# Kernel optimization log

Hardware: AMD Instinct MI355X
Metric: run time of the kernel (lower is better)

## Reference

```python
import jax, jax.numpy as jnp
import numpy as np

GN_GROUPS = 32
EPS = 1e-5
GRADIENT_MUL = 0.1
DCN_K = 3
DCN_PAD = 1


def conv(x, w, b=None, pad=0):
    out = jax.lax.conv_general_dilated(x, w, (1, 1), [(pad, pad), (pad, pad)],
                                       dimension_numbers=('NCHW', 'OIHW', 'NCHW'))
    if b is not None:
        out = out + b[None, :, None, None]
    return out


def group_norm(x, gamma, beta):
    B, C, H, W = x.shape
    xg = x.reshape(B, GN_GROUPS, C // GN_GROUPS, H, W)
    mu = xg.mean(axis=(2, 3, 4), keepdims=True)
    var = xg.var(axis=(2, 3, 4), keepdims=True)
    xg = (xg - mu) * jax.lax.rsqrt(var + EPS)
    return xg.reshape(B, C, H, W) * gamma[None, :, None, None] + beta[None, :, None, None]


def dcn_base_offset():
    base = np.arange(-DCN_PAD, DCN_PAD + 1, dtype=np.float32)
    y = np.repeat(base, DCN_K)
    x = np.tile(base, DCN_K)
    return jnp.asarray(np.stack([y, x], 1).reshape(1, -1, 1, 1))  # [1,2K,1,1], (y,x) interleaved


def deform_conv(x, offset, weight):
    # x [B,C,H,W]; offset [B,2K,H,W] (y,x) interleaved per kernel point; weight [O,C,3,3]
    B, C, H, W = x.shape
    K = DCN_K * DCN_K
    off = offset.reshape(B, K, 2, H, W)
    base = jnp.arange(DCN_K, dtype=x.dtype) - DCN_PAD
    ky = jnp.repeat(base, DCN_K)
    kx = jnp.tile(base, DCN_K)
    gy = jnp.arange(H, dtype=x.dtype)[None, None, :, None] + ky[None, :, None, None] + off[:, :, 0]
    gx = jnp.arange(W, dtype=x.dtype)[None, None, None, :] + kx[None, :, None, None] + off[:, :, 1]
    y0 = jnp.floor(gy)
    x0 = jnp.floor(gx)
    dy = gy - y0
    dx = gx - x0

    def corner(yi, xi, wgt):
        valid = (yi >= 0) & (yi < H) & (xi >= 0) & (xi < W)
        yc = jnp.clip(yi, 0, H - 1).astype(jnp.int32)
        xc = jnp.clip(xi, 0, W - 1).astype(jnp.int32)
        # gather per image: x_b[:, yc, xc] -> [C,K,H,W]
        v = jax.vmap(lambda xb, yb, xb2: xb[:, yb, xb2])(x, yc, xc)  # [B,C,K,H,W]
        return v * (wgt * valid)[:, None]

    s = (corner(y0, x0, (1 - dy) * (1 - dx)) + corner(y0, x0 + 1, (1 - dy) * dx)
         + corner(y0 + 1, x0, dy * (1 - dx)) + corner(y0 + 1, x0 + 1, dy * dx))
    wk = weight.reshape(weight.shape[0], C, K)
    return jnp.einsum('bckhw,ock->bohw', s, wk)


def setup_inputs() -> dict:
    key = jax.random.key(0)
    ks = jax.random.split(key, 10)
    B, C, H, W = 2, 256, 100, 152
    NC, PTS, S = 80, 18, 3

    def n(k, shp, std=0.01):
        return jax.random.normal(k, shp, dtype=jnp.float32) * std

    return dict(
        x=jax.random.normal(ks[0], (B, C, H, W), dtype=jnp.float32),
        cls_w=n(ks[1], (S, C, C, 3, 3)), cls_b=jnp.zeros((S, C)),
        cls_gn_g=jnp.ones((S, C)), cls_gn_b=jnp.zeros((S, C)),
        reg_w=n(ks[2], (S, C, C, 3, 3)), reg_b=jnp.zeros((S, C)),
        reg_gn_g=jnp.ones((S, C)), reg_gn_b=jnp.zeros((S, C)),
        init_conv_w=n(ks[3], (C, C, 3, 3)), init_conv_b=jnp.zeros((C,)),
        init_out_w=n(ks[4], (PTS, C, 1, 1)), init_out_b=jnp.zeros((PTS,)),
        cls_dcn_w=n(ks[5], (C, C, 3, 3)),
        cls_out_w=n(ks[6], (NC, C, 1, 1)), cls_out_b=jnp.full((NC,), -4.595, dtype=jnp.float32),
        ref_dcn_w=n(ks[7], (C, C, 3, 3)),
        ref_out_w=n(ks[8], (PTS, C, 1, 1)), ref_out_b=jnp.zeros((PTS,)),
    )


def reference(x, cls_w, cls_b, cls_gn_g, cls_gn_b, reg_w, reg_b, reg_gn_g, reg_gn_b,
              init_conv_w, init_conv_b, init_out_w, init_out_b,
              cls_dcn_w, cls_out_w, cls_out_b, ref_dcn_w, ref_out_w, ref_out_b):
    cls_feat, pts_feat = x, x
    for i in range(cls_w.shape[0]):  # stacked conv towers (conv -> GN -> ReLU)
        cls_feat = jax.nn.relu(group_norm(conv(cls_feat, cls_w[i], cls_b[i], pad=1), cls_gn_g[i], cls_gn_b[i]))
        pts_feat = jax.nn.relu(group_norm(conv(pts_feat, reg_w[i], reg_b[i], pad=1), reg_gn_g[i], reg_gn_b[i]))
    # initialize reppoints
    pts_out_init = conv(jax.nn.relu(conv(pts_feat, init_conv_w, init_conv_b, pad=1)), init_out_w, init_out_b)
    # gradient_mul trick (detach part of the gradient)
    pts_gm = GRADIENT_MUL * pts_out_init + (1.0 - GRADIENT_MUL) * jax.lax.stop_gradient(pts_out_init)
    dcn_offset = pts_gm - dcn_base_offset()
    cls_out = conv(jax.nn.relu(deform_conv(cls_feat, dcn_offset, cls_dcn_w)), cls_out_w, cls_out_b)
    pts_out_refine = conv(jax.nn.relu(deform_conv(pts_feat, dcn_offset, ref_dcn_w)), ref_out_w, ref_out_b)
    pts_out_refine = pts_out_refine + jax.lax.stop_gradient(pts_out_init)
    return cls_out, pts_out_init, pts_out_refine
```

## Files before the change

kernel.cpp:

```cpp
#include <hip/hip_runtime.h>

constexpr int B_  = 2;
constexpr int C_  = 256;
constexpr int H_  = 100;
constexpr int W_  = 152;
constexpr int HW_ = H_ * W_;
constexpr int K9 = 9;
constexpr int CK = C_ * K9;

constexpr int OFF_INIT = B_ * 80 * HW_;
constexpr int OFF_REF  = OFF_INIT + B_ * 18 * HW_;

typedef __attribute__((ext_vector_type(8))) short short8;
typedef __attribute__((ext_vector_type(4))) float f32x4;

__device__ inline unsigned short f2b(float f) {
    union { float f; unsigned u; } x; x.f = f;
    unsigned r = x.u + 0x7fff + ((x.u >> 16) & 1);
    return (unsigned short)(r >> 16);
}
__device__ inline float b2f(unsigned short b) {
    union { unsigned u; float f; } x; x.u = ((unsigned)b) << 16; return x.f;
}

__device__ inline void load_lds16(const void* g, void* l) {
    __builtin_amdgcn_global_load_lds(
        (const __attribute__((address_space(1))) unsigned int*)g,
        (__attribute__((address_space(3))) unsigned int*)l, 16, 0, 0);
}

__device__ inline int3 xcd_swizzle() {
    const int gx = gridDim.x, gxy = gridDim.x * gridDim.y;
    const int nwg = gxy * gridDim.z;
    int orig = blockIdx.x + gx * blockIdx.y + gxy * blockIdx.z;
    int q = nwg >> 3, r = nwg & 7;
    int xcd = orig & 7, idx = orig >> 3;
    int lg = (xcd < r ? xcd * (q + 1) : r * (q + 1) + (xcd - r) * q) + idx;
    int bz = lg / gxy;
    int rem = lg - bz * gxy;
    int by = rem / gx;
    int bx = rem - by * gx;
    return make_int3(bx, by, bz);
}

__global__ __launch_bounds__(256) void to_nhwc_b16_kernel(
    const float* __restrict__ in, unsigned short* __restrict__ outb)
{
    __shared__ float t[64][65];
    const int lane = threadIdx.x & 63, grp = threadIdx.x >> 6;
    const int p0 = blockIdx.x * 64;
    const int c0 = blockIdx.y * 64;
    const int b  = blockIdx.z;
#pragma unroll
    for (int j = 0; j < 16; j++) {
        int c = c0 + j * 4 + grp;
        int p = p0 + lane;
        float v = (p < HW_) ? in[((size_t)(b * C_ + c)) * HW_ + p] : 0.f;
        t[j * 4 + grp][lane] = v;
    }
    __syncthreads();
#pragma unroll
    for (int j = 0; j < 16; j++) {
        int p = p0 + j * 4 + grp;
        int c = c0 + lane;
        if (p < HW_) outb[((size_t)b * HW_ + p) * C_ + c] = f2b(t[lane][j * 4 + grp]);
    }
}

__global__ void wprep2_kernel(const float* __restrict__ w0, const float* __restrict__ w1,
                              unsigned short* __restrict__ t0, unsigned short* __restrict__ t1,
                              float* __restrict__ stats)
{
    const int co = blockIdx.x, kk = blockIdx.y, tw = blockIdx.z, ci = threadIdx.x;
    const float* w = tw ? w1 : w0;
    unsigned short* t = tw ? t1 : t0;
    t[((size_t)kk * C_ + co) * C_ + ci] = f2b(w[((size_t)co * C_ + ci) * K9 + kk]);
    if (co == 0 && kk == 0 && tw == 0) {
        stats[ci] = 0.f;
        if (ci < 32) stats[256 + ci] = 0.f;
    }
}

__global__ __launch_bounds__(256) void conv3x3_mfma8_kernel(
    const unsigned short* __restrict__ src0, const unsigned short* __restrict__ src1,
    const unsigned short* __restrict__ wtb0, const unsigned short* __restrict__ wtb1,
    const float* __restrict__ bias0, const float* __restrict__ bias1,
    unsigned short* __restrict__ dst0, unsigned short* __restrict__ dst1,
    float* __restrict__ stats, const unsigned short* __restrict__ zbuf, int relu)
{
    __shared__ __align__(16) short a_lds[2][1024 * 8];
    __shared__ __align__(16) short b_lds[2][512 * 8];

    const int3 sw = xcd_swizzle();
    const int z = sw.z, b = z & 1, ch = (z >> 1) & 1, tw = z >> 2;
    const unsigned short* act = tw ? src1 : src0;
    const unsigned short* wtb = tw ? wtb1 : wtb0;
    const float* bias = tw ? bias1 : bias0;
    unsigned short* out = tw ? dst1 : dst0;
    float* st = stats ? stats + tw * 128 : nullptr;

    const int tid = threadIdx.x;
    const int lane = tid & 63, wid = tid >> 6;
    const int wr = wid >> 1, wc = wid & 1;
    const int l15 = lane & 15, lq = lane >> 4;
    const int x0 = sw.x * 32, y0 = sw.y * 4;

    const unsigned short* sbaseA[4];
    int sstepA[4];
#pragma unroll
    for (int j = 0; j < 4; j++) {
        int p = j * 256 + tid;
        int v = p ^ ((p >> 3) & 7);
        const unsigned short* src = zbuf;
        int step = 0;
        if (v < 816) {
            int px = v >> 2, q = v & 3;
            int row = px / 34, col = px - row * 34;
            int y = y0 - 1 + row, x = x0 - 1 + col;
            if (y >= 0 && y < H_ && x >= 0 && x < W_) {
                src = act + ((size_t)(b * HW_ + y * W_ + x) * C_ + q * 8);
                step = 1;
            }
        }
        sbaseA[j] = src; sstepA[j] = step;
    }

    int boff[2];
#pragma unroll
    for (int j = 0; j < 2; j++) {
        int p = j * 256 + tid;
        int v = p ^ ((p >> 3) & 3);
        boff[j] = (v >> 2) * 256 + (v & 3) * 8;
    }

    auto STAGE_A = [&](int ci0, int bi) {
#pragma unroll
        for (int j = 0; j < 4; j++)
            load_lds16(sbaseA[j] + sstepA[j] * ci0,
                       &a_lds[bi][(size_t)(j * 256 + tid) * 8]);
    };
    auto STAGE_B = [&](int kk, int ci0, int bi) {
        const unsigned short* wb = wtb + ((size_t)kk * C_ + ch * 128) * C_ + ci0;
#pragma unroll
        for (int j = 0; j < 2; j++)
            load_lds16(wb + boff[j], &b_lds[bi][(size_t)(j * 256 + tid) * 8]);
    };

    f32x4 acc[4][4];
#pragma unroll
    for (int mf = 0; mf < 4; mf++)
#pragma unroll
        for (int nf = 0; nf < 4; nf++) acc[mf][nf] = (f32x4){0.f, 0.f, 0.f, 0.f};

    STAGE_B(0, 0, 0);
    STAGE_A(0, 0);
    asm volatile("s_waitcnt vmcnt(0)" ::: "memory");
    __builtin_amdgcn_s_barrier();

    int bbuf = 0;
    for (int c = 0; c < 8; c++) {
        const int abuf = c & 1;
        const short* ab = a_lds[abuf];
#pragma unroll
        for (int kk = 0; kk < 9; kk++) {
            int issued = 0;
            if (kk < 8)           { STAGE_B(kk + 1, c * 32, bbuf ^ 1); issued += 2; }
            else if (c < 7)       { STAGE_B(0, (c + 1) * 32, bbuf ^ 1); issued += 2; }
            if (kk == 0 && c < 7) { STAGE_A((c + 1) * 32, abuf ^ 1); issued += 4; }
            if (issued == 6)      asm volatile("s_waitcnt vmcnt(6)" ::: "memory");
            else if (issued == 2) asm volatile("s_waitcnt vmcnt(2)" ::: "memory");
            else                  asm volatile("s_waitcnt vmcnt(0)" ::: "memory");
            __builtin_amdgcn_s_barrier();

            const int ky = kk / 3, kx = kk % 3;
            short8 af[4], bf[4];
#pragma unroll
            for (int mf = 0; mf < 4; mf++) {
                int lv = ((mf + ky) * 34 + wr * 16 + l15 + kx) * 4 + lq;
                int pu = lv ^ ((lv >> 3) & 7);
                af[mf] = *(const short8*)(ab + pu * 8);
            }
            const short* bb = b_lds[bbuf];
#pragma unroll
            for (int nf = 0; nf < 4; nf++) {
                int u  = (wc * 64 + nf * 16 + l15) * 4 + lq;
                int pu = u ^ ((u >> 3) & 3);
                bf[nf] = *(const short8*)(bb + pu * 8);
            }
            __builtin_amdgcn_s_setprio(1);
#pragma unroll
            for (int nf = 0; nf < 4; nf++)
#pragma unroll
                for (int mf = 0; mf < 4; mf++)
                    acc[mf][nf] = __builtin_amdgcn_mfma_f32_16x16x32_bf16(
                        af[mf], bf[nf], acc[mf][nf], 0, 0, 0);
            __builtin_amdgcn_s_setprio(0);
            asm volatile("" ::: "memory");
            __builtin_amdgcn_s_barrier();
            asm volatile("" ::: "memory");
            bbuf ^= 1;
        }
    }

#pragma unroll
    for (int nf = 0; nf < 4; nf++) {
        int co = ch * 128 + wc * 64 + nf * 16 + l15;
        float bv = bias[co];
        float s = 0.f, ss = 0.f;
#pragma unroll
        for (int mf = 0; mf < 4; mf++) {
            int y = y0 + mf;
#pragma unroll
            for (int r = 0; r < 4; r++) {
                int x = x0 + wr * 16 + lq * 4 + r;
                if (x < W_) {
                    float v = acc[mf][nf][r] + bv;
                    s += v; ss += v * v;
                    out[((size_t)(b * HW_ + y * W_ + x)) * C_ + co] =
                        f2b(relu ? fmaxf(v, 0.f) : v);
                }
            }
        }
        if (st) {
            s  += __shfl_xor(s, 1);  ss += __shfl_xor(ss, 1);
            s  += __shfl_xor(s, 2);  ss += __shfl_xor(ss, 2);
            s  += __shfl_xor(s, 4);  ss += __shfl_xor(ss, 4);
            s  += __shfl_xor(s, 16); ss += __shfl_xor(ss, 16);
            s  += __shfl_xor(s, 32); ss += __shfl_xor(ss, 32);
            if ((lane & 55) == 0) {
                int g = co >> 3;
                atomicAdd(&st[(b * 32 + g) * 2],     s);
                atomicAdd(&st[(b * 32 + g) * 2 + 1], ss);
            }
        }
    }
}

__global__ __launch_bounds__(256) void gn2_apply_kernel(
    unsigned short* __restrict__ buf0, unsigned short* __restrict__ buf1,
    const float* __restrict__ stats,
    const float* __restrict__ g0, const float* __restrict__ be0,
    const float* __restrict__ g1, const float* __restrict__ be1)
{
    const int tw = blockIdx.y;
    unsigned short* buf = tw ? buf1 : buf0;
    const float* gamma = tw ? g1 : g0;
    const float* beta  = tw ? be1 : be0;
    const float* st = stats + tw * 128;

    const int i = blockIdx.x * 256 + threadIdx.x;
    const int c8 = i & 31;
    const int b = ((i >> 5) >= HW_) ? 1 : 0;
    const float inv_n = 1.f / (8.f * HW_);
    float s1 = st[(b * 32 + c8) * 2];
    float s2 = st[(b * 32 + c8) * 2 + 1];
    float mean = s1 * inv_n;
    float var  = s2 * inv_n - mean * mean;
    float rs = rsqrtf(var + 1e-5f);

    short8 v8 = *(const short8*)(buf + (size_t)i * 8);
    float vo[8];
#pragma unroll
    for (int j = 0; j < 8; j++) {
        int c = c8 * 8 + j;
        float ga = gamma[c] * rs;
        float be = beta[c] - mean * ga;
        vo[j] = fmaxf(fmaf(b2f((unsigned short)v8[j]), ga, be), 0.f);
    }
    unsigned pk[4];
#pragma unroll
    for (int j = 0; j < 4; j++)
        pk[j] = (unsigned)f2b(vo[2 * j]) | ((unsigned)f2b(vo[2 * j + 1]) << 16);
    *(int4*)(buf + (size_t)i * 8) = make_int4(pk[0], pk[1], pk[2], pk[3]);
}

__global__ __launch_bounds__(256) void deform3_mfma_kernel(
    const unsigned short* __restrict__ feat0, const unsigned short* __restrict__ feat1,
    const float* __restrict__ pts,
    const unsigned short* __restrict__ wtb0, const unsigned short* __restrict__ wtb1,
    unsigned short* __restrict__ out0, unsigned short* __restrict__ out1,
    const unsigned short* __restrict__ zbuf)
{
    __shared__ __align__(16) short s_lds[32 * 296];
    __shared__ __align__(16) short f_lds[512 * 8];
    __shared__ int   p_ref[288][4];
    __shared__ float p_wgt[288][4];

    const int3 sw = xcd_swizzle();
    const int z = sw.z, b = z & 1, tw = z >> 1;
    const unsigned short* feat = tw ? feat1 : feat0;
    const unsigned short* wtb  = tw ? wtb1 : wtb0;
    unsigned short* out        = tw ? out1 : out0;

    const int tid = threadIdx.x;
    const int lane = tid & 63, wc = tid >> 6;
    const int l15 = lane & 15, lq = lane >> 4;
    const int x0 = sw.x * 8, y0 = sw.y * 4;

    const unsigned short* sbase[2];
    int sstep[2];
#pragma unroll
    for (int j = 0; j < 2; j++) {
        int p = (wc + j * 4) * 64 + lane;
        int v = p ^ ((p >> 3) & 7);
        const unsigned short* src = zbuf;
        int step = 0;
        if (v < 384) {
            int pix = v >> 2, q = v & 3;
            int wy = pix / 12, wx = pix - wy * 12;
            int y = y0 - 2 + wy, x = x0 - 2 + wx;
            if (y >= 0 && y < H_ && x >= 0 && x < W_) {
                src = feat + ((size_t)(b * HW_ + y * W_ + x) * C_ + q * 8);
                step = 1;
            }
        }
        sbase[j] = src; sstep[j] = step;
    }

    for (int pr = tid; pr < 288; pr += 256) {
        int px_l = pr / 9, kk = pr - px_l * 9;
        int y = y0 + (px_l >> 3), x = x0 + (px_l & 7);
        const float* pb = pts + ((size_t)b * 18 + 2 * kk) * HW_ + y * W_ + x;
        float oy = pb[0], ox = pb[HW_];
        float gy = (float)y + oy, gx = (float)x + ox;
        float fy0 = floorf(gy), fx0 = floorf(gx);
        float dy = gy - fy0, dx = gx - fx0;
        int iy0 = (int)fy0, ix0 = (int)fx0;
        float wy2[2] = {1.f - dy, dy}, wx2[2] = {1.f - dx, dx};
#pragma unroll
        for (int cy = 0; cy < 2; cy++)
#pragma unroll
            for (int cx = 0; cx < 2; cx++) {
                int yy = iy0 + cy, xx = ix0 + cx;
                bool valid = (yy >= 0) && (yy < H_) && (xx >= 0) && (xx < W_);
                int ref = 0;
                float w = 0.f;
                if (valid) {
                    w = wy2[cy] * wx2[cx];
                    int wy = yy - (y0 - 2), wx = xx - (x0 - 2);
                    if (wy >= 0 && wy < 8 && wx >= 0 && wx < 12)
                        ref = wy * 12 + wx;
                    else
                        ref = -(int)((b * HW_ + yy * W_ + xx) * C_) - 1;
                }
                p_ref[pr][cy * 2 + cx] = ref;
                p_wgt[pr][cy * 2 + cx] = w;
            }
    }

    f32x4 acc[2][4];
#pragma unroll
    for (int mf = 0; mf < 2; mf++)
#pragma unroll
        for (int nf = 0; nf < 4; nf++) acc[mf][nf] = (f32x4){0.f, 0.f, 0.f, 0.f};

    auto STAGE = [&](int ci0) {
#pragma unroll
        for (int j = 0; j < 2; j++)
            load_lds16(sbase[j] + sstep[j] * ci0,
                       &f_lds[((wc + j * 4) * 64) * 8]);
    };

    STAGE(0);
    __syncthreads();

    for (int c = 0; c < 8; c++) {
        const int ci0 = c * 32;
        for (int u = tid; u < 1152; u += 256) {
            int q = u & 3, pr = u >> 2;
            int px_l = pr / 9, kk = pr - px_l * 9;
            int4  rf = *(const int4*)p_ref[pr];
            float4 wg = *(const float4*)p_wgt[pr];
            short8 cv[4];
            int rr[4] = {rf.x, rf.y, rf.z, rf.w};
#pragma unroll
            for (int j = 0; j < 4; j++) {
                if (rr[j] >= 0) {
                    int uu = rr[j] * 4 + q;
                    int pu = uu ^ ((uu >> 3) & 7);
                    cv[j] = *(const short8*)(f_lds + pu * 8);
                } else {
                    cv[j] = *(const short8*)(feat + (-rr[j] - 1) + ci0 + q * 8);
                }
            }
            unsigned pk[4];
#pragma unroll
            for (int j = 0; j < 4; j++) {
                float r0 = wg.x * b2f((unsigned short)cv[0][2 * j])
                         + wg.y * b2f((unsigned short)cv[1][2 * j])
                         + wg.z * b2f((unsigned short)cv[2][2 * j])
                         + wg.w * b2f((unsigned short)cv[3][2 * j]);
                float r1 = wg.x * b2f((unsigned short)cv[0][2 * j + 1])
                         + wg.y * b2f((unsigned short)cv[1][2 * j + 1])
                         + wg.z * b2f((unsigned short)cv[2][2 * j + 1])
                         + wg.w * b2f((unsigned short)cv[3][2 * j + 1]);
                asm("v_cvt_pk_bf16_f32 %0, %1, %2" : "=v"(pk[j]) : "v"(r0), "v"(r1));
            }
            *(int4*)(s_lds + px_l * 296 + kk * 32 + q * 8) = make_int4(pk[0], pk[1], pk[2], pk[3]);
        }
        __syncthreads();
        if (c < 7) STAGE(ci0 + 32);

#pragma unroll
        for (int kk = 0; kk < 9; kk++) {
            short8 af[2];
#pragma unroll
            for (int mf = 0; mf < 2; mf++)
                af[mf] = *(const short8*)(s_lds + (mf * 16 + l15) * 296 + kk * 32 + lq * 8);
#pragma unroll
            for (int nf = 0; nf < 4; nf++) {
                int co = wc * 64 + nf * 16 + l15;
                short8 bf = *(const short8*)(wtb + ((size_t)(kk * C_ + co)) * C_ + ci0 + lq * 8);
#pragma unroll
                for (int mf = 0; mf < 2; mf++)
                    acc[mf][nf] = __builtin_amdgcn_mfma_f32_16x16x32_bf16(
                        af[mf], bf, acc[mf][nf], 0, 0, 0);
            }
        }
        __syncthreads();
    }

#pragma unroll
    for (int nf = 0; nf < 4; nf++) {
        int co = wc * 64 + nf * 16 + l15;
#pragma unroll
        for (int mf = 0; mf < 2; mf++) {
#pragma unroll
            for (int r = 0; r < 4; r++) {
                int px_l = mf * 16 + lq * 4 + r;
                int y = y0 + (px_l >> 3), x = x0 + (px_l & 7);
                out[((size_t)(b * HW_ + y * W_ + x)) * C_ + co] =
                    f2b(fmaxf(acc[mf][nf][r], 0.f));
            }
        }
    }
}

template <int NOg>
__global__ __launch_bounds__(256) void conv1x1_kernel(
    const unsigned short* __restrict__ feat, const float* __restrict__ w,
    const float* __restrict__ bias, const float* __restrict__ addsrc,
    float* __restrict__ outp, int O)
{
    const int lane = threadIdx.x & 63, og = threadIdx.x >> 6;
    const int px = blockIdx.x * 64 + lane;
    const int b = (px >= HW_) ? 1 : 0;
    const int rem = px - b * HW_;
    const short8* f8 = (const short8*)(feat + (size_t)px * C_);

    float acc[NOg];
#pragma unroll
    for (int j = 0; j < NOg; j++) acc[j] = 0.f;

    for (int c8 = 0; c8 < 32; c8++) {
        short8 v8 = f8[c8];
        float vf[8];
#pragma unroll
        for (int e = 0; e < 8; e++) vf[e] = b2f((unsigned short)v8[e]);
#pragma unroll
        for (int j = 0; j < NOg; j++) {
            int o = og * NOg + j;
            if (o < O) {
                const float* wr = w + (size_t)o * C_ + c8 * 8;
                float4 w0 = *(const float4*)wr;
                float4 w1 = *(const float4*)(wr + 4);
                acc[j] = fmaf(vf[0], w0.x, acc[j]);
                acc[j] = fmaf(vf[1], w0.y, acc[j]);
                acc[j] = fmaf(vf[2], w0.z, acc[j]);
                acc[j] = fmaf(vf[3], w0.w, acc[j]);
                acc[j] = fmaf(vf[4], w1.x, acc[j]);
                acc[j] = fmaf(vf[5], w1.y, acc[j]);
                acc[j] = fmaf(vf[6], w1.z, acc[j]);
                acc[j] = fmaf(vf[7], w1.w, acc[j]);
            }
        }
    }
#pragma unroll
    for (int j = 0; j < NOg; j++) {
        int o = og * NOg + j;
        if (o < O) {
            float val = acc[j] + bias[o];
            size_t oi = ((size_t)(b * O + o)) * HW_ + rem;
            if (addsrc) val += addsrc[oi];
            outp[oi] = val;
        }
    }
}

extern "C" void kernel_launch(void* const* d_in, const int* in_sizes, int n_in,
                              void* d_out, int out_size, void* d_ws, size_t ws_size,
                              hipStream_t stream)
{
    (void)in_sizes; (void)n_in; (void)out_size; (void)ws_size;

    const float* x           = (const float*)d_in[0];
    const float* cls_w       = (const float*)d_in[1];
    const float* cls_b       = (const float*)d_in[2];
    const float* cls_gn_g    = (const float*)d_in[3];
    const float* cls_gn_b    = (const float*)d_in[4];
    const float* reg_w       = (const float*)d_in[5];
    const float* reg_b       = (const float*)d_in[6];
    const float* reg_gn_g    = (const float*)d_in[7];
    const float* reg_gn_b    = (const float*)d_in[8];
    const float* init_conv_w = (const float*)d_in[9];
    const float* init_conv_b = (const float*)d_in[10];
    const float* init_out_w  = (const float*)d_in[11];
    const float* init_out_b  = (const float*)d_in[12];
    const float* cls_dcn_w   = (const float*)d_in[13];
    const float* cls_out_w   = (const float*)d_in[14];
    const float* cls_out_b   = (const float*)d_in[15];
    const float* ref_dcn_w   = (const float*)d_in[16];
    const float* ref_out_w   = (const float*)d_in[17];
    const float* ref_out_b   = (const float*)d_in[18];

    float* out = (float*)d_out;

    const size_t NF = (size_t)B_ * C_ * HW_;
    unsigned short* xb16 = (unsigned short*)d_ws;
    unsigned short* bA   = xb16 + NF;
    unsigned short* bB   = bA + NF;
    unsigned short* bC   = bB + NF;
    unsigned short* bD   = bC + NF;
    unsigned short* wtb0 = bD + NF;
    unsigned short* wtb1 = wtb0 + (size_t)CK * C_;
    float* stats = (float*)(wtb1 + (size_t)CK * C_);
    const unsigned short* zbuf = (const unsigned short*)(stats + 256);

    const dim3 convGrid2(5, 25, 8);
    const dim3 convGrid1(5, 25, 4);
    const dim3 wprepGrid2(C_, 9, 2);
    const dim3 wprepGrid1(C_, 9, 1);
    const dim3 nhwcGrid((HW_ + 63) / 64, C_ / 64, B_);
    const dim3 gnGrid((B_ * HW_ * 32) / 256, 2);
    const dim3 deformGrid(W_ / 8, H_ / 4, 4);
    const int  px_blocks = (B_ * HW_) / 64;

    to_nhwc_b16_kernel<<<nhwcGrid, 256, 0, stream>>>(x, xb16);

    wprep2_kernel<<<wprepGrid2, 256, 0, stream>>>(cls_w, reg_w, wtb0, wtb1, stats);
    conv3x3_mfma8_kernel<<<convGrid2, 256, 0, stream>>>(
        xb16, xb16, wtb0, wtb1, cls_b, reg_b, bA, bC, stats, zbuf, 0);
    gn2_apply_kernel<<<gnGrid, 256, 0, stream>>>(
        bA, bC, stats, cls_gn_g, cls_gn_b, reg_gn_g, reg_gn_b);

    wprep2_kernel<<<wprepGrid2, 256, 0, stream>>>(
        cls_w + (size_t)C_ * CK, reg_w + (size_t)C_ * CK, wtb0, wtb1, stats);
    conv3x3_mfma8_kernel<<<convGrid2, 256, 0, stream>>>(
        bA, bC, wtb0, wtb1, cls_b + C_, reg_b + C_, bB, bD, stats, zbuf, 0);
    gn2_apply_kernel<<<gnGrid, 256, 0, stream>>>(
        bB, bD, stats, cls_gn_g + C_, cls_gn_b + C_, reg_gn_g + C_, reg_gn_b + C_);

    wprep2_kernel<<<wprepGrid2, 256, 0, stream>>>(
        cls_w + 2 * (size_t)C_ * CK, reg_w + 2 * (size_t)C_ * CK, wtb0, wtb1, stats);
    conv3x3_mfma8_kernel<<<convGrid2, 256, 0, stream>>>(
        bB, bD, wtb0, wtb1, cls_b + 2 * C_, reg_b + 2 * C_, bA, bC, stats, zbuf, 0);
    gn2_apply_kernel<<<gnGrid, 256, 0, stream>>>(
        bA, bC, stats, cls_gn_g + 2 * C_, cls_gn_b + 2 * C_,
        reg_gn_g + 2 * C_, reg_gn_b + 2 * C_);

    wprep2_kernel<<<wprepGrid1, 256, 0, stream>>>(init_conv_w, nullptr, wtb0, nullptr, stats);
    conv3x3_mfma8_kernel<<<convGrid1, 256, 0, stream>>>(
        bC, nullptr, wtb0, nullptr, init_conv_b, nullptr, bD, nullptr, nullptr, zbuf, 1);
    conv1x1_kernel<5><<<px_blocks, 256, 0, stream>>>(
        bD, init_out_w, init_out_b, nullptr, out + OFF_INIT, 18);

    wprep2_kernel<<<wprepGrid2, 256, 0, stream>>>(cls_dcn_w, ref_dcn_w, wtb0, wtb1, stats);
    deform3_mfma_kernel<<<deformGrid, 256, 0, stream>>>(
        bA, bC, out + OFF_INIT, wtb0, wtb1, bB, bD, zbuf);

    conv1x1_kernel<20><<<px_blocks, 256, 0, stream>>>(
        bB, cls_out_w, cls_out_b, nullptr, out, 80);
    conv1x1_kernel<5><<<px_blocks, 256, 0, stream>>>(
        bD, ref_out_w, ref_out_b, out + OFF_INIT, out + OFF_REF, 18);
}
```

Measured before the change: 920.0 us.

## Triple-buffer weight tiles to drop a barrier per step and fuse tail 1x1 convs

The 3x3 conv main loop now uses three B-tile LDS buffers instead of two. This removes the trailing barrier after each MFMA step and defers the next A-tile prefetch until after the barrier, so one barrier per kk step suffices. Separately, the two final 1x1 output convs are merged into one launch with a 2-row grid, removing a kernel launch and letting both run concurrently. The risks are more LDS use, which may lower occupancy, and a subtle correctness dependence on the reordered waitcnt counts.

Result: faster. 862.6 us (-6.2%).

```diff
diff --git a/kernel.cpp b/kernel.cpp
--- a/kernel.cpp
+++ b/kernel.cpp
@@ -81,7 +81,7 @@
     }
 }
 
-__global__ __launch_bounds__(256) void conv3x3_mfma8_kernel(
+__global__ __launch_bounds__(256) void conv3x3_mfma11_kernel(
     const unsigned short* __restrict__ src0, const unsigned short* __restrict__ src1,
     const unsigned short* __restrict__ wtb0, const unsigned short* __restrict__ wtb1,
     const float* __restrict__ bias0, const float* __restrict__ bias1,
@@ -89,7 +89,7 @@
     float* __restrict__ stats, const unsigned short* __restrict__ zbuf, int relu)
 {
     __shared__ __align__(16) short a_lds[2][1024 * 8];
-    __shared__ __align__(16) short b_lds[2][512 * 8];
+    __shared__ __align__(16) short b_lds[3][512 * 8];
 
     const int3 sw = xcd_swizzle();
     const int z = sw.z, b = z & 1, ch = (z >> 1) & 1, tw = z >> 2;
@@ -152,25 +152,26 @@
 #pragma unroll
         for (int nf = 0; nf < 4; nf++) acc[mf][nf] = (f32x4){0.f, 0.f, 0.f, 0.f};
 
+    STAGE_A(0, 0);
     STAGE_B(0, 0, 0);
-    STAGE_A(0, 0);
     asm volatile("s_waitcnt vmcnt(0)" ::: "memory");
     __builtin_amdgcn_s_barrier();
 
-    int bbuf = 0;
     for (int c = 0; c < 8; c++) {
         const int abuf = c & 1;
         const short* ab = a_lds[abuf];
 #pragma unroll
         for (int kk = 0; kk < 9; kk++) {
-            int issued = 0;
-            if (kk < 8)           { STAGE_B(kk + 1, c * 32, bbuf ^ 1); issued += 2; }
-            else if (c < 7)       { STAGE_B(0, (c + 1) * 32, bbuf ^ 1); issued += 2; }
-            if (kk == 0 && c < 7) { STAGE_A((c + 1) * 32, abuf ^ 1); issued += 4; }
-            if (issued == 6)      asm volatile("s_waitcnt vmcnt(6)" ::: "memory");
-            else if (issued == 2) asm volatile("s_waitcnt vmcnt(2)" ::: "memory");
-            else                  asm volatile("s_waitcnt vmcnt(0)" ::: "memory");
+            bool bIss = true;
+            if (kk < 8)      STAGE_B(kk + 1, c * 32, (kk + 1) % 3);
+            else if (c < 7)  STAGE_B(0, (c + 1) * 32, 0);
+            else             bIss = false;
+            if (kk == 1 && c < 7)  asm volatile("s_waitcnt vmcnt(6)" ::: "memory");
+            else if (bIss)         asm volatile("s_waitcnt vmcnt(2)" ::: "memory");
+            else                   asm volatile("s_waitcnt vmcnt(0)" ::: "memory");
             __builtin_amdgcn_s_barrier();
+            asm volatile("" ::: "memory");
+            if (kk == 0 && c < 7) STAGE_A((c + 1) * 32, abuf ^ 1);
 
             const int ky = kk / 3, kx = kk % 3;
             short8 af[4], bf[4];
@@ -180,7 +181,7 @@
                 int pu = lv ^ ((lv >> 3) & 7);
                 af[mf] = *(const short8*)(ab + pu * 8);
             }
-            const short* bb = b_lds[bbuf];
+            const short* bb = b_lds[kk % 3];
 #pragma unroll
             for (int nf = 0; nf < 4; nf++) {
                 int u  = (wc * 64 + nf * 16 + l15) * 4 + lq;
@@ -196,9 +197,6 @@
                         af[mf], bf[nf], acc[mf][nf], 0, 0, 0);
             __builtin_amdgcn_s_setprio(0);
             asm volatile("" ::: "memory");
-            __builtin_amdgcn_s_barrier();
-            asm volatile("" ::: "memory");
-            bbuf ^= 1;
         }
     }
 
@@ -437,7 +435,7 @@
 }
 
 template <int NOg>
-__global__ __launch_bounds__(256) void conv1x1_kernel(
+__device__ __forceinline__ void conv1x1_body(
     const unsigned short* __restrict__ feat, const float* __restrict__ w,
     const float* __restrict__ bias, const float* __restrict__ addsrc,
     float* __restrict__ outp, int O)
@@ -485,6 +483,26 @@
             outp[oi] = val;
         }
     }
+}
+
+template <int NOg>
+__global__ __launch_bounds__(256) void conv1x1_kernel(
+    const unsigned short* __restrict__ feat, const float* __restrict__ w,
+    const float* __restrict__ bias, const float* __restrict__ addsrc,
+    float* __restrict__ outp, int O)
+{
+    conv1x1_body<NOg>(feat, w, bias, addsrc, outp, O);
+}
+
+__global__ __launch_bounds__(256) void conv1x1_dual_kernel(
+    const unsigned short* __restrict__ fA, const float* __restrict__ wA,
+    const float* __restrict__ bA_, float* __restrict__ outA,
+    const unsigned short* __restrict__ fB, const float* __restrict__ wB,
+    const float* __restrict__ bB_, const float* __restrict__ addB,
+    float* __restrict__ outB)
+{
+    if (blockIdx.y == 0) conv1x1_body<20>(fA, wA, bA_, nullptr, outA, 80);
+    else                 conv1x1_body<5>(fB, wB, bB_, addB, outB, 18);
 }
 
 extern "C" void kernel_launch(void* const* d_in, const int* in_sizes, int n_in,
@@ -534,32 +552,33 @@
     const dim3 gnGrid((B_ * HW_ * 32) / 256, 2);
     const dim3 deformGrid(W_ / 8, H_ / 4, 4);
     const int  px_blocks = (B_ * HW_) / 64;
+    const dim3 tailGrid(px_blocks, 2);
 
     to_nhwc_b16_kernel<<<nhwcGrid, 256, 0, stream>>>(x, xb16);
 
     wprep2_kernel<<<wprepGrid2, 256, 0, stream>>>(cls_w, reg_w, wtb0, wtb1, stats);
-    conv3x3_mfma8_kernel<<<convGrid2, 256, 0, stream>>>(
+    conv3x3_mfma11_kernel<<<convGrid2, 256, 0, stream>>>(
         xb16, xb16, wtb0, wtb1, cls_b, reg_b, bA, bC, stats, zbuf, 0);
     gn2_apply_kernel<<<gnGrid, 256, 0, stream>>>(
         bA, bC, stats, cls_gn_g, cls_gn_b, reg_gn_g, reg_gn_b);
 
     wprep2_kernel<<<wprepGrid2, 256, 0, stream>>>(
         cls_w + (size_t)C_ * CK, reg_w + (size_t)C_ * CK, wtb0, wtb1, stats);
-    conv3x3_mfma8_kernel<<<convGrid2, 256, 0, stream>>>(
+    conv3x3_mfma11_kernel<<<convGrid2, 256, 0, stream>>>(
         bA, bC, wtb0, wtb1, cls_b + C_, reg_b + C_, bB, bD, stats, zbuf, 0);
     gn2_apply_kernel<<<gnGrid, 256, 0, stream>>>(
         bB, bD, stats, cls_gn_g + C_, cls_gn_b + C_, reg_gn_g + C_, reg_gn_b + C_);
 
     wprep2_kernel<<<wprepGrid2, 256, 0, stream>>>(
         cls_w + 2 * (size_t)C_ * CK, reg_w + 2 * (size_t)C_ * CK, wtb0, wtb1, stats);
-    conv3x3_mfma8_kernel<<<convGrid2, 256, 0, stream>>>(
+    conv3x3_mfma11_kernel<<<convGrid2, 256, 0, stream>>>(
         bB, bD, wtb0, wtb1, cls_b + 2 * C_, reg_b + 2 * C_, bA, bC, stats, zbuf, 0);
     gn2_apply_kernel<<<gnGrid, 256, 0, stream>>>(
         bA, bC, stats, cls_gn_g + 2 * C_, cls_gn_b + 2 * C_,
         reg_gn_g + 2 * C_, reg_gn_b + 2 * C_);
 
     wprep2_kernel<<<wprepGrid1, 256, 0, stream>>>(init_conv_w, nullptr, wtb0, nullptr, stats);
-    conv3x3_mfma8_kernel<<<convGrid1, 256, 0, stream>>>(
+    conv3x3_mfma11_kernel<<<convGrid1, 256, 0, stream>>>(
         bC, nullptr, wtb0, nullptr, init_conv_b, nullptr, bD, nullptr, nullptr, zbuf, 1);
     conv1x1_kernel<5><<<px_blocks, 256, 0, stream>>>(
         bD, init_out_w, init_out_b, nullptr, out + OFF_INIT, 18);
@@ -568,8 +587,7 @@
     deform3_mfma_kernel<<<deformGrid, 256, 0, stream>>>(
         bA, bC, out + OFF_INIT, wtb0, wtb1, bB, bD, zbuf);
 
-    conv1x1_kernel<20><<<px_blocks, 256, 0, stream>>>(
-        bB, cls_out_w, cls_out_b, nullptr, out, 80);
-    conv1x1_kernel<5><<<px_blocks, 256, 0, stream>>>(
-        bD, ref_out_w, ref_out_b, out + OFF_INIT, out + OFF_REF, 18);
-}
+    conv1x1_dual_kernel<<<tailGrid, 256, 0, stream>>>(
+        bB, cls_out_w, cls_out_b, out,
+        bD, ref_out_w, ref_out_b, out + OFF_INIT, out + OFF_REF);
+}
```
